# Kernel tuning notes

Measured on AMD Instinct MI355X. Metric: run time of the kernel, lower is better.

The kernel has to match this reference:

```python
import jax, jax.numpy as jnp
import numpy as np

MAX_DISTANCE = 10
N_OUT = 8


def setup_inputs() -> dict:
    key = jax.random.key(0)
    k1, k2 = jax.random.split(key)
    B, N = 32, 512
    adjacency = jax.random.uniform(k1, (B, N, N), dtype=jnp.float32)
    node_mask = jnp.ones((B, N), dtype=bool)
    emb = jax.random.normal(k2, (MAX_DISTANCE + 2, N_OUT), dtype=jnp.float32)
    return {"adjacency": adjacency, "node_mask": node_mask, "emb": emb}


def _shortest_path_indices(adjacency, node_mask):
    """All-pairs BFS distances up to MAX_DISTANCE via frontier matmuls.

    Returns int32 (B, N, N): d in [0, MAX_DISTANCE] if reachable within
    MAX_DISTANCE hops, else MAX_DISTANCE + 1 (also for invalid node pairs).
    """
    B, N, _ = adjacency.shape
    adj = adjacency > 0.5
    adj = adj | jnp.swapaxes(adj, -1, -2)  # symmetrize
    valid_pair = node_mask[:, :, None] & node_mask[:, None, :]
    adj = (adj & valid_pair).astype(jnp.float32)  # (B, N, N)

    eye = jnp.eye(N, dtype=bool)[None]
    reach0 = eye & valid_pair  # dist 0 only on valid diagonal
    dist0 = jnp.where(reach0, 0, MAX_DISTANCE + 1).astype(jnp.int32)

    def step(carry, t):
        reach, dist = carry
        expanded = jnp.matmul(reach.astype(jnp.float32), adj) > 0  # one BFS hop
        newly = expanded & ~reach
        dist = jnp.where(newly, t.astype(jnp.int32), dist)
        return (reach | newly, dist), None

    (_, dist), _ = jax.lax.scan(step, (reach0, dist0), jnp.arange(1, MAX_DISTANCE + 1))
    return dist


def reference(adjacency, node_mask, emb):
    dist = _shortest_path_indices(adjacency, node_mask)  # (B, N, N)
    return emb[dist]  # (B, N, N, n_out)
```

## Files before the change

### kernel.cpp

```cpp
#include <hip/hip_runtime.h>

#define NODES 512
#define WORDS 16
#define NBATCH 32
#define SENTINEL 11
#define NEMB 12
#define NOUT 8
#define G 4

__global__ void __launch_bounds__(256)
mask_pack(const int* __restrict__ mask, unsigned int* __restrict__ maskbits) {
    int tid = blockIdx.x * 256 + threadIdx.x;
    bool bit = mask[tid] != 0;
    unsigned long long bal = __ballot(bit);
    if ((threadIdx.x & 63) == 0) {
        int w = tid >> 5;
        maskbits[w]     = (unsigned int)bal;
        maskbits[w + 1] = (unsigned int)(bal >> 32);
    }
}

__global__ void __launch_bounds__(256)
pack_bits(const float* __restrict__ A, const int* __restrict__ mask,
          const unsigned int* __restrict__ maskbits,
          unsigned int* __restrict__ bitA) {
    int tid = blockIdx.x * 256 + threadIdx.x;
    int w = tid & 15;
    int i = (tid >> 4) & 511;
    int b = tid >> 13;
    const float4* p = (const float4*)(A + (size_t)tid * 32);
    unsigned int bits = 0;
#pragma unroll
    for (int q = 0; q < 8; ++q) {
        float4 v = p[q];
        bits |= (v.x > 0.5f ? 1u : 0u) << (4 * q);
        bits |= (v.y > 0.5f ? 1u : 0u) << (4 * q + 1);
        bits |= (v.z > 0.5f ? 1u : 0u) << (4 * q + 2);
        bits |= (v.w > 0.5f ? 1u : 0u) << (4 * q + 3);
    }
    unsigned int mw = maskbits[b * WORDS + w];
    bool rv = mask[b * NODES + i] != 0;
    bitA[tid] = rv ? (bits & mw) : 0u;
}

__global__ void __launch_bounds__(256)
symmetrize(const unsigned int* __restrict__ bitA, unsigned int* __restrict__ adjb) {
    int tid = blockIdx.x * 256 + threadIdx.x;
    int w = tid & 15;
    int i = (tid >> 4) & 511;
    int b = tid >> 13;
    const unsigned int* base = bitA + (size_t)b * NODES * WORDS;
    unsigned int word = base[i * WORDS + w];
    unsigned int t = 0;
    int iw = i >> 5, ib = i & 31;
#pragma unroll
    for (int k = 0; k < 32; ++k) {
        t |= ((base[(32 * w + k) * WORDS + iw] >> ib) & 1u) << k;
    }
    adjb[tid] = word | t;
}

__global__ void __launch_bounds__(512)
bfs_store(const unsigned int* __restrict__ adjb, const int* __restrict__ mask,
          const float* __restrict__ emb, float4* __restrict__ out4) {
    const int i0 = blockIdx.x * G;
    const int b = blockIdx.y;
    const int j = threadIdx.x;

    __shared__ unsigned int s_f[G][WORDS];
    __shared__ unsigned int s_any[8];
    __shared__ unsigned char s_dist[G][NODES];
    __shared__ __align__(16) float s_emb[NEMB * NOUT];

    if (j < NEMB * NOUT) s_emb[j] = emb[j];

    const uint4* rowp = (const uint4*)(adjb + ((size_t)b * NODES + j) * WORDS);
    unsigned int adjrow[WORDS];
    uint4 r0 = rowp[0], r1 = rowp[1], r2 = rowp[2], r3 = rowp[3];
    adjrow[0] = r0.x; adjrow[1] = r0.y; adjrow[2]  = r0.z; adjrow[3]  = r0.w;
    adjrow[4] = r1.x; adjrow[5] = r1.y; adjrow[6]  = r1.z; adjrow[7]  = r1.w;
    adjrow[8] = r2.x; adjrow[9] = r2.y; adjrow[10] = r2.z; adjrow[11] = r2.w;
    adjrow[12] = r3.x; adjrow[13] = r3.y; adjrow[14] = r3.z; adjrow[15] = r3.w;

    if (j < G * WORDS) {
        int s = j >> 4, w = j & 15;
        int i = i0 + s;
        bool v = (mask[b * NODES + i] != 0);
        s_f[s][w] = (v && (i >> 5) == w) ? (1u << (i & 31)) : 0u;
    }

    int dist[G];
    bool reach[G];
#pragma unroll
    for (int s = 0; s < G; ++s) {
        int i = i0 + s;
        bool v = (mask[b * NODES + i] != 0);
        reach[s] = (j == i) && v;
        dist[s] = reach[s] ? 0 : SENTINEL;
    }
    __syncthreads();

    for (int t = 1; t <= 10; ++t) {
        bool newly[G];
#pragma unroll
        for (int s = 0; s < G; ++s) {
            unsigned int hit = 0;
#pragma unroll
            for (int w = 0; w < WORDS; ++w) hit |= adjrow[w] & s_f[s][w];
            newly[s] = (hit != 0) && !reach[s];
        }
        __syncthreads();
        unsigned long long anyb = 0;
#pragma unroll
        for (int s = 0; s < G; ++s) {
            unsigned long long bal = __ballot(newly[s]);
            anyb |= bal;
            if ((j & 63) == 0) {
                int wv = j >> 6;
                s_f[s][2 * wv]     = (unsigned int)bal;
                s_f[s][2 * wv + 1] = (unsigned int)(bal >> 32);
            }
        }
        if ((j & 63) == 0) s_any[j >> 6] = (anyb != 0ull) ? 1u : 0u;
#pragma unroll
        for (int s = 0; s < G; ++s)
            if (newly[s]) { reach[s] = true; dist[s] = t; }
        __syncthreads();
        unsigned int any = 0;
#pragma unroll
        for (int wv = 0; wv < 8; ++wv) any |= s_any[wv];
        if (!any) break;
    }

#pragma unroll
    for (int s = 0; s < G; ++s) s_dist[s][j] = (unsigned char)dist[s];
    __syncthreads();

    const float4* e4 = (const float4*)s_emb;
#pragma unroll
    for (int s = 0; s < G; ++s) {
        size_t rb = ((size_t)b * NODES + (i0 + s)) * (NODES * NOUT / 4);
#pragma unroll
        for (int h = 0; h < 2; ++h) {
            int d = s_dist[s][(h << 8) + (j >> 1)];
            out4[rb + h * NODES + j] = e4[2 * d + (j & 1)];
        }
    }
}

extern "C" void kernel_launch(void* const* d_in, const int* in_sizes, int n_in,
                              void* d_out, int out_size, void* d_ws, size_t ws_size,
                              hipStream_t stream) {
    const float* adjacency = (const float*)d_in[0];
    const int* node_mask = (const int*)d_in[1];
    const float* emb = (const float*)d_in[2];
    float4* out4 = (float4*)d_out;

    unsigned int* maskbits = (unsigned int*)d_ws;
    unsigned int* bitA = maskbits + 512;
    unsigned int* adjb = bitA + (size_t)NBATCH * NODES * WORDS;

    mask_pack<<<64, 256, 0, stream>>>(node_mask, maskbits);
    pack_bits<<<1024, 256, 0, stream>>>(adjacency, node_mask, maskbits, bitA);
    symmetrize<<<1024, 256, 0, stream>>>(bitA, adjb);
    bfs_store<<<dim3(NODES / G, NBATCH), 512, 0, stream>>>(adjb, node_mask, emb, out4);
}
```

Baseline: 85.98 us.

## Fuse mask packing into pack_bits and double-buffer BFS frontier to drop a barrier

Folds the mask_pack kernel into pack_bits by computing the batch mask ballot in shared memory, removing one launch. The BFS loop double-buffers the frontier and state arrays so each iteration needs one __syncthreads instead of two. It also exits early once every valid node is reached, and reads the frontier as uint4 vectors. It adds a launch_bounds occupancy hint, at the cost of a redundant mask read per block in pack_bits.

```diff
diff --git a/kernel.cpp b/kernel.cpp
--- a/kernel.cpp
+++ b/kernel.cpp
@@ -9,25 +9,29 @@
 #define G 4
 
 __global__ void __launch_bounds__(256)
-mask_pack(const int* __restrict__ mask, unsigned int* __restrict__ maskbits) {
-    int tid = blockIdx.x * 256 + threadIdx.x;
-    bool bit = mask[tid] != 0;
-    unsigned long long bal = __ballot(bit);
-    if ((threadIdx.x & 63) == 0) {
-        int w = tid >> 5;
-        maskbits[w]     = (unsigned int)bal;
-        maskbits[w + 1] = (unsigned int)(bal >> 32);
+pack_bits(const float* __restrict__ A, const int* __restrict__ mask,
+          unsigned int* __restrict__ bitA) {
+    const int tid = blockIdx.x * 256 + threadIdx.x;
+    const int t = threadIdx.x;
+    const int w = tid & 15;
+    const int i = (tid >> 4) & 511;
+    const int b = tid >> 13;
+
+    __shared__ unsigned int s_mw[WORDS];
+    {
+        bool m0 = mask[b * NODES + t] != 0;
+        bool m1 = mask[b * NODES + 256 + t] != 0;
+        unsigned long long b0 = __ballot(m0);
+        unsigned long long b1 = __ballot(m1);
+        if ((t & 63) == 0) {
+            int wv = t >> 6;
+            s_mw[2 * wv]         = (unsigned int)b0;
+            s_mw[2 * wv + 1]     = (unsigned int)(b0 >> 32);
+            s_mw[8 + 2 * wv]     = (unsigned int)b1;
+            s_mw[8 + 2 * wv + 1] = (unsigned int)(b1 >> 32);
+        }
     }
-}
 
-__global__ void __launch_bounds__(256)
-pack_bits(const float* __restrict__ A, const int* __restrict__ mask,
-          const unsigned int* __restrict__ maskbits,
-          unsigned int* __restrict__ bitA) {
-    int tid = blockIdx.x * 256 + threadIdx.x;
-    int w = tid & 15;
-    int i = (tid >> 4) & 511;
-    int b = tid >> 13;
     const float4* p = (const float4*)(A + (size_t)tid * 32);
     unsigned int bits = 0;
 #pragma unroll
@@ -38,9 +42,9 @@
         bits |= (v.z > 0.5f ? 1u : 0u) << (4 * q + 2);
         bits |= (v.w > 0.5f ? 1u : 0u) << (4 * q + 3);
     }
-    unsigned int mw = maskbits[b * WORDS + w];
-    bool rv = mask[b * NODES + i] != 0;
-    bitA[tid] = rv ? (bits & mw) : 0u;
+    __syncthreads();
+    bool rv = (s_mw[i >> 5] >> (i & 31)) & 1u;
+    bitA[tid] = rv ? (bits & s_mw[w]) : 0u;
 }
 
 __global__ void __launch_bounds__(256)
@@ -60,33 +64,31 @@
     adjb[tid] = word | t;
 }
 
-__global__ void __launch_bounds__(512)
+__global__ void __launch_bounds__(512, 8)
 bfs_store(const unsigned int* __restrict__ adjb, const int* __restrict__ mask,
           const float* __restrict__ emb, float4* __restrict__ out4) {
     const int i0 = blockIdx.x * G;
     const int b = blockIdx.y;
     const int j = threadIdx.x;
 
-    __shared__ unsigned int s_f[G][WORDS];
-    __shared__ unsigned int s_any[8];
+    __shared__ unsigned int s_f[2][G][WORDS];
+    __shared__ unsigned int s_state[2][8];
     __shared__ unsigned char s_dist[G][NODES];
     __shared__ __align__(16) float s_emb[NEMB * NOUT];
 
     if (j < NEMB * NOUT) s_emb[j] = emb[j];
 
     const uint4* rowp = (const uint4*)(adjb + ((size_t)b * NODES + j) * WORDS);
-    unsigned int adjrow[WORDS];
-    uint4 r0 = rowp[0], r1 = rowp[1], r2 = rowp[2], r3 = rowp[3];
-    adjrow[0] = r0.x; adjrow[1] = r0.y; adjrow[2]  = r0.z; adjrow[3]  = r0.w;
-    adjrow[4] = r1.x; adjrow[5] = r1.y; adjrow[6]  = r1.z; adjrow[7]  = r1.w;
-    adjrow[8] = r2.x; adjrow[9] = r2.y; adjrow[10] = r2.z; adjrow[11] = r2.w;
-    adjrow[12] = r3.x; adjrow[13] = r3.y; adjrow[14] = r3.z; adjrow[15] = r3.w;
+    uint4 ar[4];
+    ar[0] = rowp[0]; ar[1] = rowp[1]; ar[2] = rowp[2]; ar[3] = rowp[3];
+
+    const bool valid_j = (mask[b * NODES + j] != 0);
 
     if (j < G * WORDS) {
         int s = j >> 4, w = j & 15;
         int i = i0 + s;
         bool v = (mask[b * NODES + i] != 0);
-        s_f[s][w] = (v && (i >> 5) == w) ? (1u << (i & 31)) : 0u;
+        s_f[0][s][w] = (v && (i >> 5) == w) ? (1u << (i & 31)) : 0u;
     }
 
     int dist[G];
@@ -94,42 +96,53 @@
 #pragma unroll
     for (int s = 0; s < G; ++s) {
         int i = i0 + s;
-        bool v = (mask[b * NODES + i] != 0);
-        reach[s] = (j == i) && v;
+        reach[s] = (j == i) && valid_j;
         dist[s] = reach[s] ? 0 : SENTINEL;
     }
     __syncthreads();
 
+    int p = 0;
     for (int t = 1; t <= 10; ++t) {
         bool newly[G];
 #pragma unroll
         for (int s = 0; s < G; ++s) {
-            unsigned int hit = 0;
-#pragma unroll
-            for (int w = 0; w < WORDS; ++w) hit |= adjrow[w] & s_f[s][w];
+            const uint4* f4 = (const uint4*)s_f[p][s];
+            uint4 f0 = f4[0], f1 = f4[1], f2 = f4[2], f3 = f4[3];
+            unsigned int hit =
+                (ar[0].x & f0.x) | (ar[0].y & f0.y) | (ar[0].z & f0.z) | (ar[0].w & f0.w) |
+                (ar[1].x & f1.x) | (ar[1].y & f1.y) | (ar[1].z & f1.z) | (ar[1].w & f1.w) |
+                (ar[2].x & f2.x) | (ar[2].y & f2.y) | (ar[2].z & f2.z) | (ar[2].w & f2.w) |
+                (ar[3].x & f3.x) | (ar[3].y & f3.y) | (ar[3].z & f3.z) | (ar[3].w & f3.w);
             newly[s] = (hit != 0) && !reach[s];
         }
-        __syncthreads();
         unsigned long long anyb = 0;
+        unsigned long long doneb = ~0ull;
 #pragma unroll
         for (int s = 0; s < G; ++s) {
             unsigned long long bal = __ballot(newly[s]);
             anyb |= bal;
+            if (newly[s]) { reach[s] = true; dist[s] = t; }
+            doneb &= __ballot(reach[s] || !valid_j);
             if ((j & 63) == 0) {
                 int wv = j >> 6;
-                s_f[s][2 * wv]     = (unsigned int)bal;
-                s_f[s][2 * wv + 1] = (unsigned int)(bal >> 32);
+                s_f[p ^ 1][s][2 * wv]     = (unsigned int)bal;
+                s_f[p ^ 1][s][2 * wv + 1] = (unsigned int)(bal >> 32);
             }
         }
-        if ((j & 63) == 0) s_any[j >> 6] = (anyb != 0ull) ? 1u : 0u;
+        if ((j & 63) == 0) {
+            s_state[p ^ 1][j >> 6] =
+                ((anyb != 0ull) ? 1u : 0u) | ((doneb == ~0ull) ? 2u : 0u);
+        }
+        __syncthreads();
+        p ^= 1;
+        unsigned int anyw = 0, donew = 2;
 #pragma unroll
-        for (int s = 0; s < G; ++s)
-            if (newly[s]) { reach[s] = true; dist[s] = t; }
-        __syncthreads();
-        unsigned int any = 0;
-#pragma unroll
-        for (int wv = 0; wv < 8; ++wv) any |= s_any[wv];
-        if (!any) break;
+        for (int wv = 0; wv < 8; ++wv) {
+            unsigned int st = s_state[p][wv];
+            anyw |= st;
+            donew &= st;
+        }
+        if (!(anyw & 1u) || (donew & 2u)) break;
     }
 
 #pragma unroll
@@ -156,12 +169,10 @@
     const float* emb = (const float*)d_in[2];
     float4* out4 = (float4*)d_out;
 
-    unsigned int* maskbits = (unsigned int*)d_ws;
-    unsigned int* bitA = maskbits + 512;
+    unsigned int* bitA = (unsigned int*)d_ws;
     unsigned int* adjb = bitA + (size_t)NBATCH * NODES * WORDS;
 
-    mask_pack<<<64, 256, 0, stream>>>(node_mask, maskbits);
-    pack_bits<<<1024, 256, 0, stream>>>(adjacency, node_mask, maskbits, bitA);
+    pack_bits<<<1024, 256, 0, stream>>>(adjacency, node_mask, bitA);
     symmetrize<<<1024, 256, 0, stream>>>(bitA, adjb);
     bfs_store<<<dim3(NODES / G, NBATCH), 512, 0, stream>>>(adjb, node_mask, emb, out4);
 }
```

After: 121.0 us. 40.8% more time.
